# Optimization experiments

Hardware: AMD Instinct MI355X
Metric: run time of the kernel (lower is better)

## Reference

```python
import jax, jax.numpy as jnp
from jax import lax
import numpy as np
import itertools

KD, NH, D, WS = 16, 8, 32, 7  # key_dim, num_heads, value dim per head, window size
SCALE = KD ** -0.5


def _affine(y, s, b):
    # eval-mode BatchNorm folded to per-channel scale/shift
    return y * s[:, None, None] + b[:, None, None]


def _conv1x1(x, w, s, b):
    return _affine(jnp.einsum('bchw,oc->bohw', x, w), s, b)


def _dwconv(x, w, s, b, pad):
    # w: (C, k, k) depthwise kernel
    y = lax.conv_general_dilated(x, w[:, None], (1, 1), [(pad, pad), (pad, pad)],
                                 feature_group_count=x.shape[1],
                                 dimension_numbers=('NCHW', 'OIHW', 'NCHW'))
    return _affine(y, s, b)


def _ffn(x, w1, s1, b1, w2, s2, b2):
    return _conv1x1(jax.nn.relu(_conv1x1(x, w1, s1, b1)), w2, s2, b2)


def _bias_idxs(res):
    pts = list(itertools.product(range(res), range(res)))
    offs, idxs = {}, []
    for p1 in pts:
        for p2 in pts:
            o = (abs(p1[0] - p2[0]), abs(p1[1] - p2[1]))
            if o not in offs:
                offs[o] = len(offs)
            idxs.append(offs[o])
    n = len(pts)
    return np.array(idxs, dtype=np.int32).reshape(n, n), len(offs)


def setup_inputs() -> dict:
    key = jax.random.key(0)
    ks = jax.random.split(key, 40)
    B, C, H, W = 128, 256, 28, 28
    hid = 2 * C
    qkv_out = 2 * KD + D  # 96
    idxs, n_off = _bias_idxs(WS)

    def w_(k, shape):
        return jax.random.normal(k, shape, jnp.float32) * 0.02

    def s_(k, c):
        return 1.0 + jax.random.normal(k, (c,), jnp.float32) * 0.05

    def b_(k, c):
        return jax.random.normal(k, (c,), jnp.float32) * 0.05

    inp = {'x': jax.random.normal(ks[0], (B, C, H, W), jnp.float32)}
    inp['dw0_w'] = w_(ks[1], (C, 3, 3)); inp['dw0_s'] = s_(ks[2], C); inp['dw0_b'] = b_(ks[3], C)
    inp['ffn0_w1'] = w_(ks[4], (hid, C)); inp['ffn0_s1'] = s_(ks[5], hid); inp['ffn0_b1'] = b_(ks[6], hid)
    inp['ffn0_w2'] = w_(ks[7], (C, hid)); inp['ffn0_s2'] = s_(ks[8], C); inp['ffn0_b2'] = b_(ks[9], C)
    inp['qkv_w'] = w_(ks[10], (NH, qkv_out, C // NH)); inp['qkv_s'] = s_(ks[11], NH * qkv_out).reshape(NH, qkv_out); inp['qkv_b'] = b_(ks[12], NH * qkv_out).reshape(NH, qkv_out)
    inp['dwq_w'] = w_(ks[13], (NH, KD, 5, 5)); inp['dwq_s'] = s_(ks[14], NH * KD).reshape(NH, KD); inp['dwq_b'] = b_(ks[15], NH * KD).reshape(NH, KD)
    inp['attn_biases'] = jax.random.normal(ks[16], (NH, n_off), jnp.float32) * 0.02
    inp['proj_w'] = w_(ks[17], (C, NH * D)); inp['proj_s'] = s_(ks[18], C); inp['proj_b'] = b_(ks[19], C)
    inp['dw1_w'] = w_(ks[20], (C, 3, 3)); inp['dw1_s'] = s_(ks[21], C); inp['dw1_b'] = b_(ks[22], C)
    inp['ffn1_w1'] = w_(ks[23], (hid, C)); inp['ffn1_s1'] = s_(ks[24], hid); inp['ffn1_b1'] = b_(ks[25], hid)
    inp['ffn1_w2'] = w_(ks[26], (C, hid)); inp['ffn1_s2'] = s_(ks[27], C); inp['ffn1_b2'] = b_(ks[28], C)
    inp['bias_idxs'] = jnp.asarray(idxs)
    return inp


def reference(x, dw0_w, dw0_s, dw0_b, ffn0_w1, ffn0_s1, ffn0_b1, ffn0_w2, ffn0_s2, ffn0_b2,
              qkv_w, qkv_s, qkv_b, dwq_w, dwq_s, dwq_b, attn_biases, proj_w, proj_s, proj_b,
              dw1_w, dw1_s, dw1_b, ffn1_w1, ffn1_s1, ffn1_b1, ffn1_w2, ffn1_s2, ffn1_b2, bias_idxs):
    B, C, H, W = x.shape
    nH, nW = H // WS, W // WS
    N = WS * WS

    x = x + _dwconv(x, dw0_w, dw0_s, dw0_b, 1)
    x = x + _ffn(x, ffn0_w1, ffn0_s1, ffn0_b1, ffn0_w2, ffn0_s2, ffn0_b2)

    # window partition: (B,C,H,W) -> (B*nH*nW, C, WS, WS)
    xw = x.reshape(B, C, nH, WS, nW, WS).transpose(0, 2, 4, 1, 3, 5).reshape(B * nH * nW, C, WS, WS)
    Bw = xw.shape[0]

    ab = attn_biases[:, bias_idxs]  # (NH, N, N)
    feats_in = xw.reshape(Bw, NH, C // NH, WS, WS)
    feat = feats_in[:, 0]
    outs = []
    for i in range(NH):
        if i > 0:
            feat = feat + feats_in[:, i]
        f = _conv1x1(feat, qkv_w[i], qkv_s[i], qkv_b[i])  # (Bw, 96, WS, WS)
        q, k, v = f[:, :KD], f[:, KD:2 * KD], f[:, 2 * KD:]
        q = _dwconv(q, dwq_w[i], dwq_s[i], dwq_b[i], 2)
        qf, kf, vf = q.reshape(Bw, KD, N), k.reshape(Bw, KD, N), v.reshape(Bw, D, N)
        attn = jnp.einsum('bdn,bdm->bnm', qf, kf) * SCALE + ab[i]
        attn = jax.nn.softmax(attn, axis=-1)
        feat = jnp.einsum('bdm,bnm->bdn', vf, attn).reshape(Bw, D, WS, WS)
        outs.append(feat)
    y = jnp.concatenate(outs, axis=1)  # (Bw, NH*D, WS, WS)
    y = _conv1x1(jax.nn.relu(y), proj_w, proj_s, proj_b)

    # window reverse
    y = y.reshape(B, nH, nW, C, WS, WS).transpose(0, 3, 1, 4, 2, 5).reshape(B, C, H, W)
    x = x + y

    x = x + _dwconv(x, dw1_w, dw1_s, dw1_b, 1)
    x = x + _ffn(x, ffn1_w1, ffn1_s1, ffn1_b1, ffn1_w2, ffn1_s2, ffn1_b2)
    return x
```

## Files before the change

### kernel.cpp

```cpp
#include <hip/hip_runtime.h>
#include <hip/hip_bf16.h>

using bf16 = __hip_bfloat16;
using short8 = __attribute__((ext_vector_type(8))) short;
using f32x4  = __attribute__((ext_vector_type(4))) float;

#define BATCH 128
#define CCH   256
#define HWSZ  784
#define NPOS  100352
#define NWIN  2048

__device__ __forceinline__ ushort f2u(float f) {
    bf16 h = __float2bfloat16(f);
    return *reinterpret_cast<ushort*>(&h);
}
__device__ __forceinline__ float u2f(ushort u) {
    bf16 h;
    *reinterpret_cast<ushort*>(&h) = u;
    return __bfloat162float(h);
}
__device__ __forceinline__ int swz64(int row, int col) {
    return row * 64 + (col ^ ((row & 7) << 3));
}
__device__ __forceinline__ void gl_lds16(const void* g, void* l) {
    __builtin_amdgcn_global_load_lds(
        (const __attribute__((address_space(1))) void*)g,
        (__attribute__((address_space(3))) void*)l, 16, 0, 0);
}

__global__ __launch_bounds__(256) void wcvt_k(const float* __restrict__ w1a,
                                              const float* __restrict__ w2a,
                                              const float* __restrict__ pw,
                                              const float* __restrict__ w1b,
                                              const float* __restrict__ w2b,
                                              const float* __restrict__ qw,
                                              const float* __restrict__ qs,
                                              const float* __restrict__ qbi,
                                              const float* __restrict__ dqw,
                                              const float* __restrict__ dqs,
                                              const float* __restrict__ dqb,
                                              ushort* __restrict__ out) {
    int i = blockIdx.x * 256 + threadIdx.x;
    if (i >= 610048) return;
    float v;
    if (i < 131072)      v = w1a[i];
    else if (i < 262144) v = w2a[i - 131072];
    else if (i < 327680) v = pw[i - 262144];
    else if (i < 458752) v = w1b[i - 327680];
    else if (i < 589824) v = w2b[i - 458752];
    else if (i < 606208) { int j = i - 589824; v = qs[j >> 5] * qw[j]; }
    else if (i < 609408) { int j = i - 606208; v = dqs[j / 25] * dqw[j]; }
    else if (i < 609920) v = qbi[i - 609408];
    else                 v = dqb[i - 609920];
    out[i] = f2u(v);
}

__global__ __launch_bounds__(256) void abx_k(const float* __restrict__ ab,
                                             const int* __restrict__ bidx,
                                             float* __restrict__ abx) {
    int i = blockIdx.x * 256 + threadIdx.x;
    if (i >= 8 * 2401) return;
    int h = i / 2401, r = i - h * 2401;
    abx[i] = ab[h * 49 + bidx[r]];
}

__global__ __launch_bounds__(256) void tin_k(const float* __restrict__ X,
                                             ushort* __restrict__ O) {
    __shared__ ushort tile[256][113];
    const int pc = blockIdx.x, b = blockIdx.y;
    const int t = threadIdx.x;
    const size_t xbase = (size_t)b * 256 * 784 + pc * 112;
    for (int r = 0; r < 112; ++r) {
        int idx = r * 256 + t;
        int c = idx / 112, p = idx - c * 112;
        tile[c][p] = f2u(X[xbase + (size_t)c * 784 + p]);
    }
    __syncthreads();
    const size_t obase = ((size_t)b * 784 + pc * 112) * 256;
    for (int r = 0; r < 112; ++r) {
        int idx = r * 256 + t;
        int p = idx >> 8, c = idx & 255;
        O[obase + (size_t)p * 256 + c] = tile[c][p];
    }
}

__global__ __launch_bounds__(256) void dw3n_k(const ushort* __restrict__ X,
                                              const float* __restrict__ Wg,
                                              const float* __restrict__ sc,
                                              const float* __restrict__ bi,
                                              ushort* __restrict__ O) {
    const int h = blockIdx.x, b = blockIdx.y;
    const int t = threadIdx.x;
    const int cg = (t & 63) << 2;
    const int wv = t >> 6;
    float wt[4][9], s[4], bb[4];
#pragma unroll
    for (int e = 0; e < 4; ++e) {
        int c = cg + e;
#pragma unroll
        for (int k = 0; k < 9; ++k) wt[e][k] = Wg[c * 9 + k];
        s[e] = sc[c]; bb[e] = bi[c];
    }
    const size_t base = (size_t)b * 784 * 256;
    for (int w = wv; w < 28; w += 4) {
        float acc[4] = {0.f, 0.f, 0.f, 0.f};
        float ctr[4] = {0.f, 0.f, 0.f, 0.f};
#pragma unroll
        for (int dh = -1; dh <= 1; ++dh) {
            int hh = h + dh;
            if (hh < 0 || hh >= 28) continue;
#pragma unroll
            for (int dw = -1; dw <= 1; ++dw) {
                int ww = w + dw;
                if (ww < 0 || ww >= 28) continue;
                uint2 xv = *(const uint2*)&X[base + (size_t)(hh * 28 + ww) * 256 + cg];
                ushort xe[4] = {(ushort)(xv.x & 0xffff), (ushort)(xv.x >> 16),
                                (ushort)(xv.y & 0xffff), (ushort)(xv.y >> 16)};
                const int k = (dh + 1) * 3 + (dw + 1);
#pragma unroll
                for (int e = 0; e < 4; ++e) {
                    float x = u2f(xe[e]);
                    if (dh == 0 && dw == 0) ctr[e] = x;
                    acc[e] += wt[e][k] * x;
                }
            }
        }
        uint2 ov;
        ushort o0 = f2u(ctr[0] + s[0] * acc[0] + bb[0]);
        ushort o1 = f2u(ctr[1] + s[1] * acc[1] + bb[1]);
        ushort o2 = f2u(ctr[2] + s[2] * acc[2] + bb[2]);
        ushort o3 = f2u(ctr[3] + s[3] * acc[3] + bb[3]);
        ov.x = (uint)o0 | ((uint)o1 << 16);
        ov.y = (uint)o2 | ((uint)o3 << 16);
        *(uint2*)&O[base + (size_t)(h * 28 + w) * 256 + cg] = ov;
    }
}

template <int NY, int IC, int OC, bool RELU_OUT, bool RESID, bool NCHW_OUT>
__global__ __launch_bounds__(256) void gemm_k(const ushort* __restrict__ X,
                                              const ushort* __restrict__ Wb,
                                              const float* __restrict__ sc,
                                              const float* __restrict__ bi,
                                              const ushort* __restrict__ res,
                                              void* __restrict__ outp) {
    __shared__ ushort As[2][128 * 32];
    __shared__ ushort Bs[2][128 * 32];
    const int t = threadIdx.x;
    constexpr int NWG = 784 * NY;
    const int lid = blockIdx.x;
    const int o = (lid & 7) * (NWG >> 3) + (lid >> 3);
    const int pos0 = (o / NY) * 128;
    const int oc0  = (o % NY) * 128;
    const int wave = t >> 6, lane = t & 63;
    const int qd = lane >> 4, ln = lane & 15;
    const int pw = (wave >> 1) * 64, ow = (wave & 1) * 64;
    const int grow = lane >> 2;
    const int gcol = ((lane & 3) ^ ((lane >> 3) & 3)) * 8;
    const int xsl = (qd ^ ((ln >> 1) & 3)) * 8;

    f32x4 acc[4][4];
#pragma unroll
    for (int i = 0; i < 4; ++i)
#pragma unroll
        for (int j = 0; j < 4; ++j) acc[i][j] = (f32x4)0.f;

    constexpr int NT = IC / 32;
#pragma unroll
    for (int r = 0; r < 2; ++r) {
        const int rowbase = wave * 16 + r * 64;
        gl_lds16(&X[(size_t)(pos0 + rowbase + grow) * IC + gcol], &As[0][rowbase * 32]);
        gl_lds16(&Wb[(size_t)(oc0 + rowbase + grow) * IC + gcol], &Bs[0][rowbase * 32]);
    }

    for (int kt = 0; kt < NT; ++kt) {
        const int cur = kt & 1;
        if (kt + 1 < NT) {
            const int k0 = (kt + 1) * 32;
#pragma unroll
            for (int r = 0; r < 2; ++r) {
                const int rowbase = wave * 16 + r * 64;
                gl_lds16(&X[(size_t)(pos0 + rowbase + grow) * IC + k0 + gcol],
                         &As[cur ^ 1][rowbase * 32]);
                gl_lds16(&Wb[(size_t)(oc0 + rowbase + grow) * IC + k0 + gcol],
                         &Bs[cur ^ 1][rowbase * 32]);
            }
            asm volatile("s_waitcnt vmcnt(4)" ::: "memory");
        } else {
            asm volatile("s_waitcnt vmcnt(0)" ::: "memory");
        }
        __builtin_amdgcn_sched_barrier(0);
        __builtin_amdgcn_s_barrier();
        __builtin_amdgcn_sched_barrier(0);

        short8 bfr[4];
#pragma unroll
        for (int j = 0; j < 4; ++j)
            bfr[j] = *(const short8*)&Bs[cur][(ow + j * 16 + ln) * 32 + xsl];
#pragma unroll
        for (int i = 0; i < 4; ++i) {
            short8 a = *(const short8*)&As[cur][(pw + i * 16 + ln) * 32 + xsl];
#pragma unroll
            for (int j = 0; j < 4; ++j)
                acc[i][j] = __builtin_amdgcn_mfma_f32_16x16x32_bf16(a, bfr[j], acc[i][j], 0, 0, 0);
        }
        __builtin_amdgcn_sched_barrier(0);
        asm volatile("s_waitcnt lgkmcnt(0)" ::: "memory");
        __builtin_amdgcn_s_barrier();
        __builtin_amdgcn_sched_barrier(0);
    }

#pragma unroll
    for (int j = 0; j < 4; ++j) {
        const int oc = oc0 + ow + j * 16 + ln;
        const float s = sc[oc], bb = bi[oc];
#pragma unroll
        for (int i = 0; i < 4; ++i) {
#pragma unroll
            for (int r = 0; r < 4; ++r) {
                const int pos = pos0 + pw + i * 16 + qd * 4 + r;
                float v = s * acc[i][j][r] + bb;
                if constexpr (RELU_OUT) v = fmaxf(v, 0.f);
                if constexpr (RESID) v += u2f(res[(size_t)pos * 256 + oc]);
                if constexpr (NCHW_OUT) {
                    int bb2 = pos / 784, hw = pos - bb2 * 784;
                    ((float*)outp)[((size_t)bb2 * 256 + oc) * 784 + hw] = v;
                } else {
                    ((ushort*)outp)[(size_t)pos * OC + oc] = f2u(v);
                }
            }
        }
    }
}

__global__ __launch_bounds__(256, 4) void attn_k(const ushort* __restrict__ X,
                                                 const ushort* __restrict__ qwb,
                                                 const ushort* __restrict__ qbb,
                                                 const ushort* __restrict__ dwvb,
                                                 const ushort* __restrict__ dbbb,
                                                 const float* __restrict__ abx,
                                                 ushort* __restrict__ Y) {
    __shared__ ushort featB[64 * 32];
    __shared__ ushort q2t[64 * 32];
    __shared__ ushort kt[64 * 32];
    __shared__ ushort vd[32 * 64];
    __shared__ ushort pt[64 * 64];
    __shared__ float  uni[16 * 121];
    __shared__ ushort dwv[3200];
    __shared__ ushort qb[512];
    __shared__ ushort dbl[128];
    __shared__ int    posmap[49];
    __shared__ int    puni[49];

    const int t = threadIdx.x;
    const int w = blockIdx.x;
    const int b = w >> 4, wh = (w >> 2) & 3, ww = w & 3;
    const int wv_ = t >> 6, lane = t & 63;
    const int ln = lane & 15, qd = lane >> 4;
    const int msl = (ln >> 1) & 3;
    const int fsl = (qd ^ msl) * 8;

    if (t < 49) {
        int pi = t / 7, pj = t - pi * 7;
        posmap[t] = b * 784 + (wh * 7 + pi) * 28 + ww * 7 + pj;
        puni[t] = (pi + 2) * 11 + (pj + 2);
    }
    for (int i = t; i < 16 * 121; i += 256) uni[i] = 0.f;
    for (int i = t; i < 64 * 32; i += 256) { q2t[i] = 0; kt[i] = 0; featB[i] = 0; }
    for (int i = t; i < 32 * 64; i += 256) vd[i] = 0;
    for (int i = t; i < 64 * 64; i += 256) pt[i] = 0;
    for (int i = t; i < 3200; i += 256) dwv[i] = dwvb[i];
    for (int i = t; i < 512; i += 256) qb[i] = qbb[i];
    if (t < 128) dbl[t] = dbbb[t];
    for (int i = t; i < 1568; i += 256) {
        int p = i >> 5, c = i & 31;
        int pi = p / 7, pj = p - pi * 7;
        featB[p * 32 + (c & 7) + (((c >> 3) ^ ((p >> 1) & 3)) << 3)] =
            X[(size_t)(b * 784 + (wh * 7 + pi) * 28 + ww * 7 + pj) * 256 + c];
    }
    __syncthreads();

    const int arow = (16 * wv_ + ln) * 32 + fsl;

    for (int head = 0; head < 8; ++head) {
        {
            short8 afr = *(const short8*)&qwb[head * 2048 + (16 * wv_ + ln) * 32 + qd * 8];
            f32x4 acc[4];
#pragma unroll
            for (int j = 0; j < 4; ++j) acc[j] = (f32x4)0.f;
#pragma unroll
            for (int j = 0; j < 4; ++j) {
                short8 bfr = *(const short8*)&featB[(16 * j + ln) * 32 + fsl];
                acc[j] = __builtin_amdgcn_mfma_f32_16x16x32_bf16(afr, bfr, acc[j], 0, 0, 0);
            }
            float qbv[4];
#pragma unroll
            for (int r = 0; r < 4; ++r)
                qbv[r] = u2f(qb[head * 64 + 16 * wv_ + qd * 4 + r]);
#pragma unroll
            for (int j = 0; j < 4; ++j) {
                int p = 16 * j + ln;
                if (p >= 49) continue;
                if (wv_ == 0) {
                    int pu = puni[p];
#pragma unroll
                    for (int r = 0; r < 4; ++r)
                        uni[(qd * 4 + r) * 121 + pu] = acc[j][r] + qbv[r];
                } else if (wv_ == 1) {
#pragma unroll
                    for (int r = 0; r < 4; ++r)
                        kt[p * 32 + ((qd * 4 + r) & 7) + ((((qd >> 1)) ^ msl) << 3)] =
                            f2u(acc[j][r] + qbv[r]);
                } else {
#pragma unroll
                    for (int r = 0; r < 4; ++r)
                        vd[swz64((wv_ - 2) * 16 + qd * 4 + r, p)] =
                            f2u(acc[j][r] + qbv[r]);
                }
            }
        }
        __syncthreads();

        {
            const int d = ln;
            float tap[25];
#pragma unroll
            for (int u = 0; u < 25; ++u)
                tap[u] = u2f(dwv[head * 400 + d * 25 + u]);
            float db = u2f(dbl[head * 16 + d]);
#pragma unroll
            for (int k = 0; k < 4; ++k) {
                int p = 16 * wv_ + k * 4 + qd;
                int mq = (2 * k + (qd >> 1)) & 3;
                if (p < 49) {
                    const float* qp = &uni[d * 121 + (puni[p] - 24)];
                    float a = 0.f;
#pragma unroll
                    for (int u = 0; u < 5; ++u)
#pragma unroll
                        for (int v5 = 0; v5 < 5; ++v5)
                            a += tap[u * 5 + v5] * qp[u * 11 + v5];
                    q2t[p * 32 + (d & 7) + (((d >> 3) ^ mq) << 3)] = f2u(a + db);
                }
            }
        }

        {
            short8 afr = *(const short8*)&q2t[arow];
            f32x4 acc[4];
#pragma unroll
            for (int j = 0; j < 4; ++j) acc[j] = (f32x4)0.f;
#pragma unroll
            for (int j = 0; j < 4; ++j) {
                short8 bfr = *(const short8*)&kt[(16 * j + ln) * 32 + fsl];
                acc[j] = __builtin_amdgcn_mfma_f32_16x16x32_bf16(afr, bfr, acc[j], 0, 0, 0);
            }
            const int nbase = 16 * wv_ + qd * 4;
            float lg[4][4];
#pragma unroll
            for (int j = 0; j < 4; ++j) {
                int m = 16 * j + ln;
#pragma unroll
                for (int r = 0; r < 4; ++r) {
                    int n = nbase + r;
                    if (n < 49 && m < 49)
                        lg[j][r] = acc[j][r] * 0.25f + abx[head * 2401 + n * 49 + m];
                    else
                        lg[j][r] = -3e38f;
                }
            }
            float mx[4], sm[4];
#pragma unroll
            for (int r = 0; r < 4; ++r)
                mx[r] = fmaxf(fmaxf(lg[0][r], lg[1][r]), fmaxf(lg[2][r], lg[3][r]));
#pragma unroll
            for (int s = 1; s <= 8; s <<= 1)
#pragma unroll
                for (int r = 0; r < 4; ++r)
                    mx[r] = fmaxf(mx[r], __shfl_xor(mx[r], s, 16));
#pragma unroll
            for (int r = 0; r < 4; ++r) sm[r] = 0.f;
#pragma unroll
            for (int j = 0; j < 4; ++j) {
                int m = 16 * j + ln;
#pragma unroll
                for (int r = 0; r < 4; ++r) {
                    float e = __expf(lg[j][r] - mx[r]);
                    sm[r] += e;
                    int n = nbase + r;
                    if (n < 49 && m < 49) pt[swz64(n, m)] = f2u(e);
                }
            }
#pragma unroll
            for (int s = 1; s <= 8; s <<= 1)
#pragma unroll
                for (int r = 0; r < 4; ++r)
                    sm[r] += __shfl_xor(sm[r], s, 16);
            float inv[4];
#pragma unroll
            for (int r = 0; r < 4; ++r) inv[r] = 1.f / sm[r];

            f32x4 av[2];
            av[0] = (f32x4)0.f; av[1] = (f32x4)0.f;
#pragma unroll
            for (int ks = 0; ks < 2; ++ks) {
                const int cs = (ks * 32 + qd * 8) ^ ((ln & 7) << 3);
                short8 pa = *(const short8*)&pt[(16 * wv_ + ln) * 64 + cs];
#pragma unroll
                for (int dt = 0; dt < 2; ++dt) {
                    short8 vb = *(const short8*)&vd[(16 * dt + ln) * 64 + cs];
                    av[dt] = __builtin_amdgcn_mfma_f32_16x16x32_bf16(pa, vb, av[dt], 0, 0, 0);
                }
            }
#pragma unroll
            for (int r = 0; r < 4; ++r) {
                int n = nbase + r;
                if (n >= 49) continue;
                size_t pbase = (size_t)posmap[n] * 256;
                int mn = (2 * qd + (r >> 1)) & 3;
#pragma unroll
                for (int dt = 0; dt < 2; ++dt) {
                    int c = 16 * dt + ln;
                    float val = av[dt][r] * inv[r];
                    Y[pbase + head * 32 + c] = f2u(fmaxf(val, 0.f));
                    if (head < 7)
                        featB[n * 32 + (ln & 7) +
                              (((2 * dt + (ln >> 3)) ^ mn) << 3)] =
                            f2u(val + u2f(X[pbase + (head + 1) * 32 + c]));
                }
            }
        }
        __syncthreads();
    }
}

extern "C" void kernel_launch(void* const* d_in, const int* in_sizes, int n_in,
                              void* d_out, int out_size, void* d_ws, size_t ws_size,
                              hipStream_t stream) {
    const float* x       = (const float*)d_in[0];
    const float* dw0_w   = (const float*)d_in[1];
    const float* dw0_s   = (const float*)d_in[2];
    const float* dw0_b   = (const float*)d_in[3];
    const float* ffn0_w1 = (const float*)d_in[4];
    const float* ffn0_s1 = (const float*)d_in[5];
    const float* ffn0_b1 = (const float*)d_in[6];
    const float* ffn0_w2 = (const float*)d_in[7];
    const float* ffn0_s2 = (const float*)d_in[8];
    const float* ffn0_b2 = (const float*)d_in[9];
    const float* qkv_w   = (const float*)d_in[10];
    const float* qkv_s   = (const float*)d_in[11];
    const float* qkv_b   = (const float*)d_in[12];
    const float* dwq_w   = (const float*)d_in[13];
    const float* dwq_s   = (const float*)d_in[14];
    const float* dwq_b   = (const float*)d_in[15];
    const float* attn_b  = (const float*)d_in[16];
    const float* proj_w  = (const float*)d_in[17];
    const float* proj_s  = (const float*)d_in[18];
    const float* proj_b  = (const float*)d_in[19];
    const float* dw1_w   = (const float*)d_in[20];
    const float* dw1_s   = (const float*)d_in[21];
    const float* dw1_b   = (const float*)d_in[22];
    const float* ffn1_w1 = (const float*)d_in[23];
    const float* ffn1_s1 = (const float*)d_in[24];
    const float* ffn1_b1 = (const float*)d_in[25];
    const float* ffn1_w2 = (const float*)d_in[26];
    const float* ffn1_s2 = (const float*)d_in[27];
    const float* ffn1_b2 = (const float*)d_in[28];
    const int*   bidx    = (const int*)d_in[29];

    char* ws = (char*)d_ws;
    const size_t NEL = (size_t)NPOS * 256;
    ushort* wbf = (ushort*)ws;
    float*  abx = (float*)(ws + 1220096);
    ushort* U0 = (ushort*)(ws + 1220096 + 76832);
    ushort* U1 = U0 + NEL;
    ushort* U2 = U1 + NEL;
    ushort* H  = U2 + NEL;
    const ushort* w1a_b = wbf;
    const ushort* w2a_b = wbf + 131072;
    const ushort* prj_b = wbf + 262144;
    const ushort* w1b_b = wbf + 327680;
    const ushort* w2b_b = wbf + 458752;
    const ushort* qwb   = wbf + 589824;
    const ushort* dwvb  = wbf + 606208;
    const ushort* qbb   = wbf + 609408;
    const ushort* dbbb  = wbf + 609920;

    wcvt_k<<<2383, 256, 0, stream>>>(ffn0_w1, ffn0_w2, proj_w, ffn1_w1, ffn1_w2,
                                     qkv_w, qkv_s, qkv_b, dwq_w, dwq_s, dwq_b, wbf);
    abx_k<<<76, 256, 0, stream>>>(attn_b, bidx, abx);
    tin_k<<<dim3(7, BATCH), 256, 0, stream>>>(x, U0);
    dw3n_k<<<dim3(28, BATCH), 256, 0, stream>>>(U0, dw0_w, dw0_s, dw0_b, U1);
    gemm_k<4, 256, 512, true, false, false>
        <<<3136, 256, 0, stream>>>(U1, w1a_b, ffn0_s1, ffn0_b1, nullptr, H);
    gemm_k<2, 512, 256, false, true, false>
        <<<1568, 256, 0, stream>>>(H, w2a_b, ffn0_s2, ffn0_b2, U1, U2);
    attn_k<<<NWIN, 256, 0, stream>>>(U2, qwb, qbb, dwvb, dbbb, abx, U0);
    gemm_k<2, 256, 256, false, true, false>
        <<<1568, 256, 0, stream>>>(U0, prj_b, proj_s, proj_b, U2, U1);
    dw3n_k<<<dim3(28, BATCH), 256, 0, stream>>>(U1, dw1_w, dw1_s, dw1_b, U2);
    gemm_k<4, 256, 512, true, false, false>
        <<<3136, 256, 0, stream>>>(U2, w1b_b, ffn1_s1, ffn1_b1, nullptr, H);
    gemm_k<2, 512, 256, false, true, true>
        <<<1568, 256, 0, stream>>>(H, w2b_b, ffn1_s2, ffn1_b2, U2, d_out);
}
```

Baseline: 847.1 us.

## Fuse FFN up- and down-projection GEMMs into one kernel keeping hidden in LDS

Replaces each pair of FFN GEMM launches with a single kernel that computes a 64-position tile's hidden activations in 128-channel chunks, stores them in LDS, and immediately accumulates the down-projection. This removes the global-memory round trip of the 512-channel hidden tensor and one launch per FFN. In exchange, weights are read straight from global memory for every tile without LDS staging, the kernel uses about 48KB of LDS per block which limits occupancy, and barriers sit between the two phases.

```diff
diff --git a/kernel.cpp b/kernel.cpp
--- a/kernel.cpp
+++ b/kernel.cpp
@@ -230,6 +230,108 @@
                 }
             }
         }
+    }
+}
+
+template <bool NCHW_OUT>
+__global__ __launch_bounds__(256) void ffn_k(const ushort* __restrict__ X,
+                                             const ushort* __restrict__ W1,
+                                             const float* __restrict__ s1,
+                                             const float* __restrict__ b1,
+                                             const ushort* __restrict__ W2,
+                                             const float* __restrict__ s2,
+                                             const float* __restrict__ b2,
+                                             const ushort* __restrict__ res,
+                                             void* __restrict__ outp) {
+    __shared__ ushort Xs[64 * 256];
+    __shared__ ushort Hs[64 * 128];
+    const int t = threadIdx.x;
+    const int pos0 = blockIdx.x * 64;
+    const int wv = t >> 6, lane = t & 63;
+    const int qd = lane >> 4, ln = lane & 15;
+    const int sl = (qd ^ ((ln >> 1) & 3)) * 8;
+
+#pragma unroll
+    for (int g = 0; g < 8; ++g) {
+        const int ub = (wv + g * 4) * 512;
+        const int row = 2 * (wv + g * 4) + (lane >> 5);
+        const int chunk = (lane & 31) >> 2;
+        const int lslot = (lane & 3) ^ ((row >> 1) & 3);
+        gl_lds16(&X[(size_t)(pos0 + row) * 256 + chunk * 32 + lslot * 8], &Xs[ub]);
+    }
+    __syncthreads();
+
+    f32x4 acc2[4][4];
+#pragma unroll
+    for (int i = 0; i < 4; ++i)
+#pragma unroll
+        for (int j = 0; j < 4; ++j) acc2[i][j] = (f32x4)0.f;
+
+    for (int hc = 0; hc < 4; ++hc) {
+        f32x4 acc1[4][2];
+#pragma unroll
+        for (int i = 0; i < 4; ++i) { acc1[i][0] = (f32x4)0.f; acc1[i][1] = (f32x4)0.f; }
+#pragma unroll
+        for (int kk = 0; kk < 8; ++kk) {
+            short8 bf0 = *(const short8*)&W1[(size_t)(hc * 128 + wv * 32 + ln) * 256 + kk * 32 + qd * 8];
+            short8 bf1 = *(const short8*)&W1[(size_t)(hc * 128 + wv * 32 + 16 + ln) * 256 + kk * 32 + qd * 8];
+#pragma unroll
+            for (int i = 0; i < 4; ++i) {
+                short8 a = *(const short8*)&Xs[(i * 16 + ln) * 256 + kk * 32 + sl];
+                acc1[i][0] = __builtin_amdgcn_mfma_f32_16x16x32_bf16(a, bf0, acc1[i][0], 0, 0, 0);
+                acc1[i][1] = __builtin_amdgcn_mfma_f32_16x16x32_bf16(a, bf1, acc1[i][1], 0, 0, 0);
+            }
+        }
+#pragma unroll
+        for (int j = 0; j < 2; ++j) {
+            const int hl = wv * 32 + j * 16 + ln;
+            const float s = s1[hc * 128 + hl], bb = b1[hc * 128 + hl];
+            const int chunk = hl >> 5, slot = (hl >> 3) & 3, e = hl & 7;
+#pragma unroll
+            for (int i = 0; i < 4; ++i)
+#pragma unroll
+                for (int r = 0; r < 4; ++r) {
+                    const int p = i * 16 + qd * 4 + r;
+                    float v = fmaxf(s * acc1[i][j][r] + bb, 0.f);
+                    Hs[p * 128 + chunk * 32 + ((slot ^ ((p >> 1) & 3)) << 3) + e] = f2u(v);
+                }
+        }
+        __syncthreads();
+
+#pragma unroll
+        for (int kc = 0; kc < 4; ++kc) {
+            short8 b2f[4];
+#pragma unroll
+            for (int j = 0; j < 4; ++j)
+                b2f[j] = *(const short8*)&W2[(size_t)(wv * 64 + j * 16 + ln) * 512 + hc * 128 + kc * 32 + qd * 8];
+#pragma unroll
+            for (int i = 0; i < 4; ++i) {
+                short8 a = *(const short8*)&Hs[(i * 16 + ln) * 128 + kc * 32 + sl];
+#pragma unroll
+                for (int j = 0; j < 4; ++j)
+                    acc2[i][j] = __builtin_amdgcn_mfma_f32_16x16x32_bf16(a, b2f[j], acc2[i][j], 0, 0, 0);
+            }
+        }
+        __syncthreads();
+    }
+
+#pragma unroll
+    for (int j = 0; j < 4; ++j) {
+        const int oc = wv * 64 + j * 16 + ln;
+        const float s = s2[oc], bb = b2[oc];
+#pragma unroll
+        for (int i = 0; i < 4; ++i)
+#pragma unroll
+            for (int r = 0; r < 4; ++r) {
+                const int pos = pos0 + i * 16 + qd * 4 + r;
+                float v = s * acc2[i][j][r] + bb + u2f(res[(size_t)pos * 256 + oc]);
+                if constexpr (NCHW_OUT) {
+                    int bb2 = pos / 784, hw = pos - bb2 * 784;
+                    ((float*)outp)[((size_t)bb2 * 256 + oc) * 784 + hw] = v;
+                } else {
+                    ((ushort*)outp)[(size_t)pos * 256 + oc] = f2u(v);
+                }
+            }
     }
 }
 
@@ -476,6 +578,7 @@
     ushort* U1 = U0 + NEL;
     ushort* U2 = U1 + NEL;
     ushort* H  = U2 + NEL;
+    (void)H;
     const ushort* w1a_b = wbf;
     const ushort* w2a_b = wbf + 131072;
     const ushort* prj_b = wbf + 262144;
@@ -491,16 +594,12 @@
     abx_k<<<76, 256, 0, stream>>>(attn_b, bidx, abx);
     tin_k<<<dim3(7, BATCH), 256, 0, stream>>>(x, U0);
     dw3n_k<<<dim3(28, BATCH), 256, 0, stream>>>(U0, dw0_w, dw0_s, dw0_b, U1);
-    gemm_k<4, 256, 512, true, false, false>
-        <<<3136, 256, 0, stream>>>(U1, w1a_b, ffn0_s1, ffn0_b1, nullptr, H);
-    gemm_k<2, 512, 256, false, true, false>
-        <<<1568, 256, 0, stream>>>(H, w2a_b, ffn0_s2, ffn0_b2, U1, U2);
+    ffn_k<false><<<1568, 256, 0, stream>>>(U1, w1a_b, ffn0_s1, ffn0_b1,
+                                           w2a_b, ffn0_s2, ffn0_b2, U1, U2);
     attn_k<<<NWIN, 256, 0, stream>>>(U2, qwb, qbb, dwvb, dbbb, abx, U0);
     gemm_k<2, 256, 256, false, true, false>
         <<<1568, 256, 0, stream>>>(U0, prj_b, proj_s, proj_b, U2, U1);
     dw3n_k<<<dim3(28, BATCH), 256, 0, stream>>>(U1, dw1_w, dw1_s, dw1_b, U2);
-    gemm_k<4, 256, 512, true, false, false>
-        <<<3136, 256, 0, stream>>>(U2, w1b_b, ffn1_s1, ffn1_b1, nullptr, H);
-    gemm_k<2, 512, 256, false, true, true>
-        <<<1568, 256, 0, stream>>>(H, w2b_b, ffn1_s2, ffn1_b2, U2, d_out);
-}
+    ffn_k<true><<<1568, 256, 0, stream>>>(U2, w1b_b, ffn1_s1, ffn1_b1,
+                                          w2b_b, ffn1_s2, ffn1_b2, U2, d_out);
+}
```

New measurement: 914.6 us. 1.08x slower.
